# Optimization experiments

Measured on AMD Instinct MI355X. Metric: run time of the kernel, lower is better.

Reference implementation:

```python
import jax, jax.numpy as jnp
import numpy as np

N = 50000      # total nodes
G = 100        # graphs in batch
NPG = N // G   # nodes per graph (contiguous)
E = 800000     # total edges (avg degree 16)
F_IN = 256
HID = 128
C = 4


def setup_inputs() -> dict:
    key = jax.random.key(0)
    ks = jax.random.split(key, 16)
    w = lambda k, shape: (jax.random.normal(k, shape, dtype=jnp.float32) * 0.02)
    x = jax.random.normal(ks[0], (N, F_IN), dtype=jnp.float32)
    # edges within graphs: pick a graph per edge, then local src/dst
    g = jax.random.randint(ks[1], (E,), 0, G, dtype=jnp.int32)
    src = g * NPG + jax.random.randint(ks[2], (E,), 0, NPG, dtype=jnp.int32)
    dst = g * NPG + jax.random.randint(ks[3], (E,), 0, NPG, dtype=jnp.int32)
    edge_index = jnp.stack([src, dst], axis=0)
    batch = jnp.repeat(jnp.arange(G, dtype=jnp.int32), NPG)
    return {
        "x": x,
        "edge_index": edge_index,
        "batch": batch,
        "num_graphs": G,
        "W_bu1": w(ks[4], (F_IN, HID)), "b_bu1": jnp.zeros((HID,), jnp.float32),
        "W_td1": w(ks[5], (F_IN, HID)), "b_td1": jnp.zeros((HID,), jnp.float32),
        "W_bu2": w(ks[6], (F_IN + HID, HID)), "b_bu2": jnp.zeros((HID,), jnp.float32),
        "W_td2": w(ks[7], (F_IN + HID, HID)), "b_td2": jnp.zeros((HID,), jnp.float32),
        "W_lin": w(ks[8], (2 * HID, C)), "b_lin": jnp.zeros((C,), jnp.float32),
    }


def _gcn(h_in, src, dst, W, b, n):
    """PyG GCNConv: sym-normalized aggregation with self loops, then bias."""
    h = h_in @ W                                        # [N, H]
    # deg = in-degree at dst + 1 (self loop)
    deg = jnp.ones((n,), h.dtype).at[dst].add(jnp.ones(src.shape, h.dtype))
    dinv = jax.lax.rsqrt(deg)                           # [N]
    coef = (dinv[src] * dinv[dst])[:, None]             # [E, 1]
    agg = jnp.zeros_like(h).at[dst].add(h[src] * coef)  # scatter-add messages
    agg = agg + h * (dinv * dinv)[:, None]              # self-loop term
    return agg + b


def reference(x, edge_index, batch, num_graphs,
              W_bu1, b_bu1, W_td1, b_td1,
              W_bu2, b_bu2, W_td2, b_td2,
              W_lin, b_lin):
    n = x.shape[0]
    g = num_graphs
    src, dst = edge_index[0], edge_index[1]  # top-down direction
    # root = first node index of each (contiguous) graph
    root = jax.ops.segment_min(jnp.arange(n), batch, num_segments=g)  # [G]
    root_full = x[root][batch]                                        # repeat_interleave of root feats
    # layer 1: bottom-up uses flipped edges, top-down uses edges as-is
    l1_bu = _gcn(x, dst, src, W_bu1, b_bu1, n)
    l1_td = _gcn(x, src, dst, W_td1, b_td1, n)
    cb = jax.nn.relu(jnp.concatenate([root_full, l1_bu], axis=-1))  # dropout is identity in eval
    ct = jax.nn.relu(jnp.concatenate([root_full, l1_td], axis=-1))
    # layer 2: original code passes the top-down edge_index to BOTH convs
    l2_bu = jax.nn.relu(_gcn(cb, src, dst, W_bu2, b_bu2, n))
    l2_td = jax.nn.relu(_gcn(ct, src, dst, W_td2, b_td2, n))
    # repeat root rows over each graph then segment-mean == the root row itself
    pb = l2_bu[root]   # [G, HID]
    pt = l2_td[root]   # [G, HID]
    total = jnp.concatenate([pb, pt], axis=-1)          # [G, 2*HID]
    return jax.nn.log_softmax(total @ W_lin + b_lin, axis=-1)
```

## Files before the change

### kernel.cpp

```cpp
#include <hip/hip_runtime.h>
#include <math.h>

constexpr int F_IN = 256;
constexpr int HID  = 128;
constexpr int CLS  = 4;

constexpr int SMAX  = 2560;
constexpr int ECAP  = 64;
constexpr int QCAP  = 512;
constexpr int GMAX  = 128;

__global__ void k_setup(int* __restrict__ sidx, int* __restrict__ slist,
                        int* __restrict__ counters,
                        int* __restrict__ cnt_bu, int* __restrict__ cnt_td,
                        int* __restrict__ qcur, int* __restrict__ cur_bu,
                        int* __restrict__ cur_td, int N, int G, int NPG) {
  int i = blockIdx.x * blockDim.x + threadIdx.x;
  if (i == 0) counters[0] = G;
  if (i < GMAX) qcur[i] = 0;
  if (i < SMAX) { cur_bu[i] = 0; cur_td[i] = 0; }
  if (i >= N) return;
  cnt_bu[i] = 0;
  cnt_td[i] = 0;
  int g = i / NPG;
  bool isroot = (i - g * NPG) == 0;
  sidx[i] = isroot ? g : -1;
  if (isroot) slist[g] = i;
}

__global__ void k_claim(const int* __restrict__ src, const int* __restrict__ dst,
                        int* __restrict__ sidx, int* __restrict__ slist,
                        int* __restrict__ qbuf, int* __restrict__ qcur,
                        int* __restrict__ counters, int E, int NPG) {
  int i = blockIdx.x * blockDim.x + threadIdx.x;
  int e0 = i * 4;
  int dv[4];
  int ne = 0;
  if (e0 + 3 < E) {
    int4 d4 = ((const int4*)dst)[i];
    dv[0] = d4.x; dv[1] = d4.y; dv[2] = d4.z; dv[3] = d4.w;
    ne = 4;
  } else {
    for (int e = e0; e < E; ++e) dv[ne++] = dst[e];
  }
#pragma unroll
  for (int k = 0; k < 4; ++k) {
    if (k >= ne) break;
    int d = dv[k];
    int dg = d / NPG;
    if (d - dg * NPG == 0) {
      int s = src[e0 + k];
      int p = atomicAdd(&qcur[dg], 1);
      if (p < QCAP) qbuf[dg * QCAP + p] = s;
      if (atomicCAS(&sidx[s], -1, -2) == -1) {
        int slot = atomicAdd(&counters[0], 1);
        if (slot < SMAX) { slist[slot] = s; sidx[s] = slot; }
        else sidx[s] = -1;
      }
    }
  }
}

__global__ void k_degfill(const int* __restrict__ src, const int* __restrict__ dst,
                          const int* __restrict__ sidx,
                          int* __restrict__ cnt_bu, int* __restrict__ cnt_td,
                          int* __restrict__ cur_bu, int* __restrict__ cur_td,
                          int* __restrict__ ebuf_bu, int* __restrict__ ebuf_td,
                          int E) {
  int i = blockIdx.x * blockDim.x + threadIdx.x;
  int e0 = i * 4;
  int sv[4], dv[4];
  int ne = 0;
  if (e0 + 3 < E) {
    int4 s4 = ((const int4*)src)[i];
    int4 d4 = ((const int4*)dst)[i];
    sv[0] = s4.x; sv[1] = s4.y; sv[2] = s4.z; sv[3] = s4.w;
    dv[0] = d4.x; dv[1] = d4.y; dv[2] = d4.z; dv[3] = d4.w;
    ne = 4;
  } else {
    for (int e = e0; e < E; ++e) { sv[ne] = src[e]; dv[ne] = dst[e]; ++ne; }
  }
#pragma unroll
  for (int k = 0; k < 4; ++k) {
    if (k >= ne) break;
    int s = sv[k], d = dv[k];
    atomicAdd(&cnt_bu[s], 1);
    atomicAdd(&cnt_td[d], 1);
    int ss = sidx[s];
    if (ss >= 0) { int p = atomicAdd(&cur_bu[ss], 1); if (p < ECAP) ebuf_bu[ss * ECAP + p] = d; }
    int sd = sidx[d];
    if (sd >= 0) { int p = atomicAdd(&cur_td[sd], 1); if (p < ECAP) ebuf_td[sd * ECAP + p] = s; }
  }
}

__global__ __launch_bounds__(1024) void k_gl1(
    const float* __restrict__ x, const int* __restrict__ slist,
    const int* __restrict__ counters,
    const int* __restrict__ cnt_bu, const int* __restrict__ cnt_td,
    const int* __restrict__ ebuf_bu, const int* __restrict__ ebuf_td,
    const float* __restrict__ Wbu, const float* __restrict__ bbu,
    const float* __restrict__ Wtd, const float* __restrict__ btd,
    float* __restrict__ l1_bu, float* __restrict__ l1_td) {
  constexpr int TS = 8;
  __shared__ float zb[TS][F_IN];
  __shared__ float zt[TS][F_IN];
  int scnt = min(counters[0], SMAX);
  int base = blockIdx.x * TS;
  if (base >= scnt) return;
  int ns = min(TS, scnt - base);
  int tid = threadIdx.x, lane = tid & 63, wv = tid >> 6;
  {
    int sl = wv & 7;
    bool td = wv >= 8;
    if (sl < ns) {
      const int* cnt = td ? cnt_td : cnt_bu;
      const int* eb  = (td ? ebuf_td : ebuf_bu) + (base + sl) * ECAP;
      int u = slist[base + sl];
      int dg = cnt[u];
      int m = min(dg, ECAP);
      float ax = 0.f, ay = 0.f, az = 0.f, aw = 0.f;
      for (int j = 0; j < m; ++j) {
        int node = eb[j];
        float dv = rsqrtf(1.f + (float)cnt[node]);
        float4 v = ((const float4*)x)[(size_t)node * 64 + lane];
        ax += dv * v.x; ay += dv * v.y; az += dv * v.z; aw += dv * v.w;
      }
      float du = rsqrtf(1.f + (float)dg);
      float4 xv = ((const float4*)x)[(size_t)u * 64 + lane];
      float* zrow = td ? zt[sl] : zb[sl];
      zrow[lane * 4 + 0] = du * ax + du * du * xv.x;
      zrow[lane * 4 + 1] = du * ay + du * du * xv.y;
      zrow[lane * 4 + 2] = du * az + du * du * xv.z;
      zrow[lane * 4 + 3] = du * aw + du * du * xv.w;
    }
  }
  __syncthreads();
  int h256 = tid & 255;
  int sgrp = tid >> 8;
  bool isbu = (h256 < HID);
  int h = isbu ? h256 : h256 - HID;
  const float* W = isbu ? Wbu : Wtd;
  const float (*Z)[F_IN] = isbu ? zb : zt;
  int t0 = sgrp * 2, t1 = sgrp * 2 + 1;
  float a0 = 0.f, a1 = 0.f;
  for (int f = 0; f < F_IN; ++f) {
    float wvv = W[f * HID + h];
    a0 += Z[t0][f] * wvv;
    a1 += Z[t1][f] * wvv;
  }
  float bias = isbu ? bbu[h] : btd[h];
  float* outp = isbu ? l1_bu : l1_td;
  if (t0 < ns) outp[(size_t)(base + t0) * HID + h] = a0 + bias;
  if (t1 < ns) outp[(size_t)(base + t1) * HID + h] = a1 + bias;
}

__global__ void k_out(const float* __restrict__ x,
                      const int* __restrict__ sidx, const int* __restrict__ cnt_td,
                      const int* __restrict__ qbuf, const int* __restrict__ qcur,
                      const float* __restrict__ l1_bu, const float* __restrict__ l1_td,
                      const float* __restrict__ Wbu2, const float* __restrict__ bbu2,
                      const float* __restrict__ Wtd2, const float* __restrict__ btd2,
                      const float* __restrict__ Wlin, const float* __restrict__ blin,
                      float* __restrict__ out, int G, int NPG) {
  __shared__ int   s_slot[QCAP + 1];
  __shared__ float s_coef[QCAP + 1];
  __shared__ float front[F_IN];
  __shared__ float av[2 * HID];
  __shared__ float total[2 * HID];
  __shared__ float logits[CLS];
  int g = blockIdx.x;
  int tid = threadIdx.x;
  int r = g * NPG;
  int nq = min(qcur[g], QCAP);
  int items = nq + 1;
  float dr = rsqrtf(1.f + (float)cnt_td[r]);
  for (int i = tid; i < items; i += 256) {
    int s = (i < nq) ? qbuf[g * QCAP + i] : r;
    s_slot[i] = sidx[s];
    s_coef[i] = rsqrtf(1.f + (float)cnt_td[s]) * dr;
  }
  __syncthreads();
  bool isbu = (tid < HID);
  int h = isbu ? tid : tid - HID;
  const float* l1v = isbu ? l1_bu : l1_td;
  float acc = 0.f, csum = 0.f;
  for (int i = 0; i < items; ++i) {
    float c = s_coef[i];
    csum += c;
    int slot = s_slot[i];
    if (slot >= 0) acc += c * fmaxf(l1v[(size_t)slot * HID + h], 0.f);
  }
  av[tid]    = acc;
  front[tid] = csum * fmaxf(x[(size_t)r * F_IN + tid], 0.f);
  __syncthreads();
  const float* W  = isbu ? Wbu2 : Wtd2;
  const float* ah = isbu ? av : (av + HID);
  float acc2 = isbu ? bbu2[h] : btd2[h];
  for (int f = 0; f < F_IN; ++f) acc2 += front[f] * W[f * HID + h];
  for (int j = 0; j < HID; ++j)  acc2 += ah[j] * W[(F_IN + j) * HID + h];
  total[tid] = fmaxf(acc2, 0.f);
  __syncthreads();
  if (tid < CLS) {
    float a = blin[tid];
    for (int k = 0; k < 2 * HID; ++k) a += total[k] * Wlin[k * CLS + tid];
    logits[tid] = a;
  }
  __syncthreads();
  if (tid < CLS) {
    float m = logits[0];
    for (int c = 1; c < CLS; ++c) m = fmaxf(m, logits[c]);
    float se = 0.f;
    for (int c = 0; c < CLS; ++c) se += expf(logits[c] - m);
    out[(size_t)g * CLS + tid] = logits[tid] - m - logf(se);
  }
}

extern "C" void kernel_launch(void* const* d_in, const int* in_sizes, int n_in,
                              void* d_out, int out_size, void* d_ws, size_t ws_size,
                              hipStream_t stream) {
  const float* x    = (const float*)d_in[0];
  const int*  eidx  = (const int*)d_in[1];
  const float* Wbu1 = (const float*)d_in[4];
  const float* bbu1 = (const float*)d_in[5];
  const float* Wtd1 = (const float*)d_in[6];
  const float* btd1 = (const float*)d_in[7];
  const float* Wbu2 = (const float*)d_in[8];
  const float* bbu2 = (const float*)d_in[9];
  const float* Wtd2 = (const float*)d_in[10];
  const float* btd2 = (const float*)d_in[11];
  const float* Wlin = (const float*)d_in[12];
  const float* blin = (const float*)d_in[13];
  float* out = (float*)d_out;

  int N = in_sizes[2];
  int E = in_sizes[1] / 2;
  int G = out_size / CLS;
  int NPG = N / G;
  const int* src = eidx;
  const int* dst = eidx + E;

  char* p = (char*)d_ws;
  auto alloc = [&](size_t bytes) -> char* {
    char* r = p; p += (bytes + 255) & ~(size_t)255; return r;
  };
  int*   counters  = (int*)  alloc(64);
  int*   cnt_bu    = (int*)  alloc((size_t)N * 4);
  int*   cnt_td    = (int*)  alloc((size_t)N * 4);
  int*   qcur      = (int*)  alloc((size_t)GMAX * 4);
  int*   cur_bu    = (int*)  alloc((size_t)SMAX * 4);
  int*   cur_td    = (int*)  alloc((size_t)SMAX * 4);
  int*   sidx      = (int*)  alloc((size_t)N * 4);
  int*   slist     = (int*)  alloc((size_t)SMAX * 4);
  int*   qbuf      = (int*)  alloc((size_t)GMAX * QCAP * 4);
  int*   ebuf_bu   = (int*)  alloc((size_t)SMAX * ECAP * 4);
  int*   ebuf_td   = (int*)  alloc((size_t)SMAX * ECAP * 4);
  float* l1_bu     = (float*)alloc((size_t)SMAX * HID * 4);
  float* l1_td     = (float*)alloc((size_t)SMAX * HID * 4);

  const int T = 256;
  int quarter = (E + 3) / 4;
  k_setup  <<<(N + T - 1) / T, T, 0, stream>>>(sidx, slist, counters,
                                               cnt_bu, cnt_td, qcur, cur_bu, cur_td,
                                               N, G, NPG);
  k_claim  <<<(quarter + T - 1) / T, T, 0, stream>>>(src, dst, sidx, slist,
                                                     qbuf, qcur, counters, E, NPG);
  k_degfill<<<(quarter + T - 1) / T, T, 0, stream>>>(src, dst, sidx,
                                                     cnt_bu, cnt_td, cur_bu, cur_td,
                                                     ebuf_bu, ebuf_td, E);
  k_gl1    <<<(SMAX + 7) / 8, 1024, 0, stream>>>(x, slist, counters, cnt_bu, cnt_td,
                                                 ebuf_bu, ebuf_td,
                                                 Wbu1, bbu1, Wtd1, btd1, l1_bu, l1_td);
  k_out    <<<G, T, 0, stream>>>(x, sidx, cnt_td, qbuf, qcur,
                                 l1_bu, l1_td, Wbu2, bbu2, Wtd2, btd2,
                                 Wlin, blin, out, G, NPG);
}
```

Baseline: 254.0 us.

## Fuse layer-1 GCN computation into per-graph output kernel

Merges the layer-1 kernel (k_gl1) into the final per-graph kernel, so each graph's block computes layer-1 features for its root's in-neighbours in chunks of 16 and accumulates them straight into the layer-2 aggregate. This drops one kernel launch and the l1 intermediate buffers and slist. Root slots are now claimed inside k_claim instead of being preassigned. The trade-off is that layer-1 work now runs on only G=100 blocks of 1024 threads instead of one block per 8 slots, which reduces parallelism. Neighbours shared between graphs are no longer deduplicated, so a node feeding two graphs is computed twice.

```diff
diff --git a/kernel.cpp b/kernel.cpp
--- a/kernel.cpp
+++ b/kernel.cpp
@@ -9,30 +9,35 @@
 constexpr int ECAP  = 64;
 constexpr int QCAP  = 512;
 constexpr int GMAX  = 128;
-
-__global__ void k_setup(int* __restrict__ sidx, int* __restrict__ slist,
-                        int* __restrict__ counters,
+constexpr int CH    = 16;
+
+__global__ void k_setup(int* __restrict__ sidx,
                         int* __restrict__ cnt_bu, int* __restrict__ cnt_td,
                         int* __restrict__ qcur, int* __restrict__ cur_bu,
-                        int* __restrict__ cur_td, int N, int G, int NPG) {
+                        int* __restrict__ cur_td, int* __restrict__ counters,
+                        int N) {
   int i = blockIdx.x * blockDim.x + threadIdx.x;
-  if (i == 0) counters[0] = G;
+  if (i == 0) counters[0] = 0;
   if (i < GMAX) qcur[i] = 0;
   if (i < SMAX) { cur_bu[i] = 0; cur_td[i] = 0; }
   if (i >= N) return;
   cnt_bu[i] = 0;
   cnt_td[i] = 0;
-  int g = i / NPG;
-  bool isroot = (i - g * NPG) == 0;
-  sidx[i] = isroot ? g : -1;
-  if (isroot) slist[g] = i;
+  sidx[i] = -1;
 }
 
 __global__ void k_claim(const int* __restrict__ src, const int* __restrict__ dst,
-                        int* __restrict__ sidx, int* __restrict__ slist,
+                        int* __restrict__ sidx,
                         int* __restrict__ qbuf, int* __restrict__ qcur,
-                        int* __restrict__ counters, int E, int NPG) {
+                        int* __restrict__ counters, int E, int G, int NPG) {
   int i = blockIdx.x * blockDim.x + threadIdx.x;
+  if (i < G) {
+    int v = i * NPG;
+    if (atomicCAS(&sidx[v], -1, -2) == -1) {
+      int slot = atomicAdd(&counters[0], 1);
+      sidx[v] = (slot < SMAX) ? slot : -1;
+    }
+  }
   int e0 = i * 4;
   int dv[4];
   int ne = 0;
@@ -54,8 +59,7 @@
       if (p < QCAP) qbuf[dg * QCAP + p] = s;
       if (atomicCAS(&sidx[s], -1, -2) == -1) {
         int slot = atomicAdd(&counters[0], 1);
-        if (slot < SMAX) { slist[slot] = s; sidx[s] = slot; }
-        else sidx[s] = -1;
+        sidx[s] = (slot < SMAX) ? slot : -1;
       }
     }
   }
@@ -93,112 +97,126 @@
   }
 }
 
-__global__ __launch_bounds__(1024) void k_gl1(
-    const float* __restrict__ x, const int* __restrict__ slist,
-    const int* __restrict__ counters,
+__global__ __launch_bounds__(1024) void k_outF(
+    const float* __restrict__ x, const int* __restrict__ sidx,
     const int* __restrict__ cnt_bu, const int* __restrict__ cnt_td,
+    const int* __restrict__ qbuf, const int* __restrict__ qcur,
     const int* __restrict__ ebuf_bu, const int* __restrict__ ebuf_td,
-    const float* __restrict__ Wbu, const float* __restrict__ bbu,
-    const float* __restrict__ Wtd, const float* __restrict__ btd,
-    float* __restrict__ l1_bu, float* __restrict__ l1_td) {
-  constexpr int TS = 8;
-  __shared__ float zb[TS][F_IN];
-  __shared__ float zt[TS][F_IN];
-  int scnt = min(counters[0], SMAX);
-  int base = blockIdx.x * TS;
-  if (base >= scnt) return;
-  int ns = min(TS, scnt - base);
-  int tid = threadIdx.x, lane = tid & 63, wv = tid >> 6;
-  {
-    int sl = wv & 7;
-    bool td = wv >= 8;
-    if (sl < ns) {
-      const int* cnt = td ? cnt_td : cnt_bu;
-      const int* eb  = (td ? ebuf_td : ebuf_bu) + (base + sl) * ECAP;
-      int u = slist[base + sl];
-      int dg = cnt[u];
-      int m = min(dg, ECAP);
-      float ax = 0.f, ay = 0.f, az = 0.f, aw = 0.f;
-      for (int j = 0; j < m; ++j) {
-        int node = eb[j];
-        float dv = rsqrtf(1.f + (float)cnt[node]);
-        float4 v = ((const float4*)x)[(size_t)node * 64 + lane];
-        ax += dv * v.x; ay += dv * v.y; az += dv * v.z; aw += dv * v.w;
-      }
-      float du = rsqrtf(1.f + (float)dg);
-      float4 xv = ((const float4*)x)[(size_t)u * 64 + lane];
-      float* zrow = td ? zt[sl] : zb[sl];
-      zrow[lane * 4 + 0] = du * ax + du * du * xv.x;
-      zrow[lane * 4 + 1] = du * ay + du * du * xv.y;
-      zrow[lane * 4 + 2] = du * az + du * du * xv.z;
-      zrow[lane * 4 + 3] = du * aw + du * du * xv.w;
-    }
-  }
-  __syncthreads();
-  int h256 = tid & 255;
-  int sgrp = tid >> 8;
-  bool isbu = (h256 < HID);
-  int h = isbu ? h256 : h256 - HID;
-  const float* W = isbu ? Wbu : Wtd;
-  const float (*Z)[F_IN] = isbu ? zb : zt;
-  int t0 = sgrp * 2, t1 = sgrp * 2 + 1;
-  float a0 = 0.f, a1 = 0.f;
-  for (int f = 0; f < F_IN; ++f) {
-    float wvv = W[f * HID + h];
-    a0 += Z[t0][f] * wvv;
-    a1 += Z[t1][f] * wvv;
-  }
-  float bias = isbu ? bbu[h] : btd[h];
-  float* outp = isbu ? l1_bu : l1_td;
-  if (t0 < ns) outp[(size_t)(base + t0) * HID + h] = a0 + bias;
-  if (t1 < ns) outp[(size_t)(base + t1) * HID + h] = a1 + bias;
-}
-
-__global__ void k_out(const float* __restrict__ x,
-                      const int* __restrict__ sidx, const int* __restrict__ cnt_td,
-                      const int* __restrict__ qbuf, const int* __restrict__ qcur,
-                      const float* __restrict__ l1_bu, const float* __restrict__ l1_td,
-                      const float* __restrict__ Wbu2, const float* __restrict__ bbu2,
-                      const float* __restrict__ Wtd2, const float* __restrict__ btd2,
-                      const float* __restrict__ Wlin, const float* __restrict__ blin,
-                      float* __restrict__ out, int G, int NPG) {
-  __shared__ int   s_slot[QCAP + 1];
-  __shared__ float s_coef[QCAP + 1];
+    const float* __restrict__ Wbu1, const float* __restrict__ bbu1,
+    const float* __restrict__ Wtd1, const float* __restrict__ btd1,
+    const float* __restrict__ Wbu2, const float* __restrict__ bbu2,
+    const float* __restrict__ Wtd2, const float* __restrict__ btd2,
+    const float* __restrict__ Wlin, const float* __restrict__ blin,
+    float* __restrict__ out, int G, int NPG) {
+  __shared__ float zz[CH][2][F_IN];
+  __shared__ int   s_item[CH];
+  __shared__ int   s_slot[CH];
+  __shared__ float s_coef[CH];
+  __shared__ float av[2 * HID];
+  __shared__ float p4[4][2 * HID];
   __shared__ float front[F_IN];
-  __shared__ float av[2 * HID];
   __shared__ float total[2 * HID];
   __shared__ float logits[CLS];
+  __shared__ float s_csum;
+
   int g = blockIdx.x;
   int tid = threadIdx.x;
   int r = g * NPG;
   int nq = min(qcur[g], QCAP);
   int items = nq + 1;
   float dr = rsqrtf(1.f + (float)cnt_td[r]);
-  for (int i = tid; i < items; i += 256) {
-    int s = (i < nq) ? qbuf[g * QCAP + i] : r;
-    s_slot[i] = sidx[s];
-    s_coef[i] = rsqrtf(1.f + (float)cnt_td[s]) * dr;
-  }
-  __syncthreads();
-  bool isbu = (tid < HID);
-  int h = isbu ? tid : tid - HID;
-  const float* l1v = isbu ? l1_bu : l1_td;
-  float acc = 0.f, csum = 0.f;
-  for (int i = 0; i < items; ++i) {
-    float c = s_coef[i];
-    csum += c;
-    int slot = s_slot[i];
-    if (slot >= 0) acc += c * fmaxf(l1v[(size_t)slot * HID + h], 0.f);
-  }
-  av[tid]    = acc;
-  front[tid] = csum * fmaxf(x[(size_t)r * F_IN + tid], 0.f);
-  __syncthreads();
-  const float* W  = isbu ? Wbu2 : Wtd2;
-  const float* ah = isbu ? av : (av + HID);
-  float acc2 = isbu ? bbu2[h] : btd2[h];
-  for (int f = 0; f < F_IN; ++f) acc2 += front[f] * W[f * HID + h];
-  for (int j = 0; j < HID; ++j)  acc2 += ah[j] * W[(F_IN + j) * HID + h];
-  total[tid] = fmaxf(acc2, 0.f);
+  if (tid < 2 * HID) av[tid] = 0.f;
+  if (tid == 0) s_csum = 0.f;
+
+  for (int base = 0; base < items; base += CH) {
+    int nc = min(CH, items - base);
+    __syncthreads();
+    if (tid < nc) {
+      int it = base + tid;
+      int s = (it < nq) ? qbuf[g * QCAP + it] : r;
+      s_item[tid] = s;
+      s_slot[tid] = sidx[s];
+      s_coef[tid] = rsqrtf(1.f + (float)cnt_td[s]) * dr;
+    }
+    __syncthreads();
+    {
+      int lane = tid & 63, wv = tid >> 6;
+      for (int u = wv; u < 2 * CH; u += 16) {
+        int il = u & (CH - 1);
+        int dir = u >> 4;
+        if (il >= nc) continue;
+        int s = s_item[il], slot = s_slot[il];
+        const int* cnt = dir ? cnt_td : cnt_bu;
+        int dg = cnt[s];
+        float a0 = 0.f, a1 = 0.f, a2 = 0.f, a3 = 0.f;
+        if (slot >= 0) {
+          const int* eb = (dir ? ebuf_td : ebuf_bu) + (size_t)slot * ECAP;
+          int m = min(dg, ECAP);
+          for (int j = 0; j < m; ++j) {
+            int node = eb[j];
+            float dv = rsqrtf(1.f + (float)cnt[node]);
+            float4 v = ((const float4*)x)[(size_t)node * 64 + lane];
+            a0 += dv * v.x; a1 += dv * v.y; a2 += dv * v.z; a3 += dv * v.w;
+          }
+        }
+        float du = rsqrtf(1.f + (float)dg);
+        float4 xv = ((const float4*)x)[(size_t)s * 64 + lane];
+        float* zr = &zz[il][dir][lane * 4];
+        zr[0] = du * a0 + du * du * xv.x;
+        zr[1] = du * a1 + du * du * xv.y;
+        zr[2] = du * a2 + du * du * xv.z;
+        zr[3] = du * a3 + du * du * xv.w;
+      }
+    }
+    __syncthreads();
+    {
+      int h256 = tid & 255, ig = tid >> 8;
+      int dir = (h256 >= HID) ? 1 : 0;
+      int h = h256 & (HID - 1);
+      const float* W1 = dir ? Wtd1 : Wbu1;
+      const float* b1 = dir ? btd1 : bbu1;
+      float part = 0.f;
+      for (int k = 0; k < CH / 4; ++k) {
+        int il = ig + k * 4;
+        if (il >= nc) break;
+        float a = b1[h];
+        const float* zr = zz[il][dir];
+        for (int f = 0; f < F_IN; ++f) a += zr[f] * W1[f * HID + h];
+        part += s_coef[il] * fmaxf(a, 0.f);
+      }
+      p4[ig][h256] = part;
+    }
+    __syncthreads();
+    if (tid < 2 * HID) av[tid] += p4[0][tid] + p4[1][tid] + p4[2][tid] + p4[3][tid];
+    if (tid == 0) {
+      float cs = 0.f;
+      for (int i2 = 0; i2 < nc; ++i2) cs += s_coef[i2];
+      s_csum += cs;
+    }
+  }
+  __syncthreads();
+  if (tid < F_IN) front[tid] = s_csum * fmaxf(x[(size_t)r * F_IN + tid], 0.f);
+  __syncthreads();
+  {
+    int h256 = tid & 255, ig = tid >> 8;
+    int dir = (h256 >= HID) ? 1 : 0;
+    int h = h256 & (HID - 1);
+    const float* W2 = dir ? Wtd2 : Wbu2;
+    const float* avd = dir ? (av + HID) : av;
+    float part = 0.f;
+    for (int f = ig * 96; f < ig * 96 + 96; ++f) {
+      float v = (f < F_IN) ? front[f] : avd[f - F_IN];
+      part += v * W2[f * HID + h];
+    }
+    p4[ig][h256] = part;
+  }
+  __syncthreads();
+  if (tid < 2 * HID) {
+    int dir = (tid >= HID) ? 1 : 0;
+    int h = tid & (HID - 1);
+    float b2 = dir ? btd2[h] : bbu2[h];
+    total[tid] = fmaxf(p4[0][tid] + p4[1][tid] + p4[2][tid] + p4[3][tid] + b2, 0.f);
+  }
   __syncthreads();
   if (tid < CLS) {
     float a = blin[tid];
@@ -243,34 +261,29 @@
   auto alloc = [&](size_t bytes) -> char* {
     char* r = p; p += (bytes + 255) & ~(size_t)255; return r;
   };
-  int*   counters  = (int*)  alloc(64);
-  int*   cnt_bu    = (int*)  alloc((size_t)N * 4);
-  int*   cnt_td    = (int*)  alloc((size_t)N * 4);
-  int*   qcur      = (int*)  alloc((size_t)GMAX * 4);
-  int*   cur_bu    = (int*)  alloc((size_t)SMAX * 4);
-  int*   cur_td    = (int*)  alloc((size_t)SMAX * 4);
-  int*   sidx      = (int*)  alloc((size_t)N * 4);
-  int*   slist     = (int*)  alloc((size_t)SMAX * 4);
-  int*   qbuf      = (int*)  alloc((size_t)GMAX * QCAP * 4);
-  int*   ebuf_bu   = (int*)  alloc((size_t)SMAX * ECAP * 4);
-  int*   ebuf_td   = (int*)  alloc((size_t)SMAX * ECAP * 4);
-  float* l1_bu     = (float*)alloc((size_t)SMAX * HID * 4);
-  float* l1_td     = (float*)alloc((size_t)SMAX * HID * 4);
+  int* counters = (int*)alloc(64);
+  int* cnt_bu   = (int*)alloc((size_t)N * 4);
+  int* cnt_td   = (int*)alloc((size_t)N * 4);
+  int* qcur     = (int*)alloc((size_t)GMAX * 4);
+  int* cur_bu   = (int*)alloc((size_t)SMAX * 4);
+  int* cur_td   = (int*)alloc((size_t)SMAX * 4);
+  int* sidx     = (int*)alloc((size_t)N * 4);
+  int* qbuf     = (int*)alloc((size_t)GMAX * QCAP * 4);
+  int* ebuf_bu  = (int*)alloc((size_t)SMAX * ECAP * 4);
+  int* ebuf_td  = (int*)alloc((size_t)SMAX * ECAP * 4);
 
   const int T = 256;
   int quarter = (E + 3) / 4;
-  k_setup  <<<(N + T - 1) / T, T, 0, stream>>>(sidx, slist, counters,
-                                               cnt_bu, cnt_td, qcur, cur_bu, cur_td,
-                                               N, G, NPG);
-  k_claim  <<<(quarter + T - 1) / T, T, 0, stream>>>(src, dst, sidx, slist,
-                                                     qbuf, qcur, counters, E, NPG);
+  k_setup  <<<(N + T - 1) / T, T, 0, stream>>>(sidx, cnt_bu, cnt_td, qcur,
+                                               cur_bu, cur_td, counters, N);
+  k_claim  <<<(quarter + T - 1) / T, T, 0, stream>>>(src, dst, sidx, qbuf, qcur,
+                                                     counters, E, G, NPG);
   k_degfill<<<(quarter + T - 1) / T, T, 0, stream>>>(src, dst, sidx,
                                                      cnt_bu, cnt_td, cur_bu, cur_td,
                                                      ebuf_bu, ebuf_td, E);
-  k_gl1    <<<(SMAX + 7) / 8, 1024, 0, stream>>>(x, slist, counters, cnt_bu, cnt_td,
-                                                 ebuf_bu, ebuf_td,
-                                                 Wbu1, bbu1, Wtd1, btd1, l1_bu, l1_td);
-  k_out    <<<G, T, 0, stream>>>(x, sidx, cnt_td, qbuf, qcur,
-                                 l1_bu, l1_td, Wbu2, bbu2, Wtd2, btd2,
-                                 Wlin, blin, out, G, NPG);
-}
+  k_outF   <<<G, 1024, 0, stream>>>(x, sidx, cnt_bu, cnt_td, qbuf, qcur,
+                                    ebuf_bu, ebuf_td,
+                                    Wbu1, bbu1, Wtd1, btd1,
+                                    Wbu2, bbu2, Wtd2, btd2,
+                                    Wlin, blin, out, G, NPG);
+}
```

After: 301.6 us. 1.19x slower.
